# Kernel optimization log

Measured on AMD Instinct MI355X. Metric: run time of the kernel, lower is better.

The kernel has to match this reference:

```python
import jax, jax.numpy as jnp
import numpy as np

H = 16          # heads_num
D = 1024        # model_dim
HD = D // H     # per-head dim
NEG = -1e9


def setup_inputs() -> dict:
    key = jax.random.key(0)
    ks = jax.random.split(key, 12)
    B, S = 4, 1024
    inp = {
        "q": jax.random.normal(ks[0], (B, S, D), jnp.float32),
        "k": jax.random.normal(ks[1], (B, S, D), jnp.float32),
        "v": jax.random.normal(ks[2], (B, S, D), jnp.float32),
        "mask": jnp.ones((B, 1, S), jnp.int32),
    }
    s = 1.0 / np.sqrt(D)
    inp["Wq"] = jax.random.normal(ks[3], (D, D), jnp.float32) * s
    inp["bq"] = jnp.zeros((D,), jnp.float32)
    inp["Wk"] = jax.random.normal(ks[4], (D, D), jnp.float32) * s
    inp["bk"] = jnp.zeros((D,), jnp.float32)
    inp["Wv"] = jax.random.normal(ks[5], (D, D), jnp.float32) * s
    inp["bv"] = jnp.zeros((D,), jnp.float32)
    inp["Wo"] = jax.random.normal(ks[6], (D, D), jnp.float32) * s
    inp["bo"] = jnp.zeros((D,), jnp.float32)
    return inp


def _split_heads(x, B):
    # [B, S, D] -> [B, H, S, HD]
    return x.reshape(B, -1, H, HD).transpose(0, 2, 1, 3)


def reference(q, k, v, mask, Wq, bq, Wk, bk, Wv, bv, Wo, bo):
    B = q.shape[0]
    qh = _split_heads(q @ Wq.T + bq, B)  # [B,H,Sq,HD]
    kh = _split_heads(k @ Wk.T + bk, B)  # [B,H,Sk,HD]
    vh = _split_heads(v @ Wv.T + bv, B)  # [B,H,Sk,HD]
    scores = jnp.einsum("bhqd,bhkd->bhqk", qh, kh) / np.sqrt(HD)
    # mask [B,1,Sk] -> unsqueeze head dim -> [B,1,1,Sk], broadcast over q and heads
    scores = jnp.where(mask[:, None] == 0, NEG, scores)
    attn = jax.nn.softmax(scores, axis=-1)  # dropout in eval mode = identity
    ctx = jnp.einsum("bhqk,bhkd->bhqd", attn, vh)
    out = ctx.transpose(0, 2, 1, 3).reshape(B, -1, D)
    return out @ Wo.T + bo
```

## Files before the change

kernel.cpp:

```cpp
#include <hip/hip_runtime.h>
#include <hip/hip_bf16.h>
#include <math.h>

typedef __bf16 bf16;
typedef __bf16 bf16x8 __attribute__((ext_vector_type(8)));
typedef __bf16 bf16x2 __attribute__((ext_vector_type(2)));
typedef float f32x4 __attribute__((ext_vector_type(4)));
typedef float f32x16 __attribute__((ext_vector_type(16)));

#define D_MODEL 1024
#define SEQ 1024
#define BATCH 4
#define NHEAD 16
#define MTOT (BATCH*SEQ)

#define QSCALE 0.18033688011112042f
#define MASKNEG -1e9f

__global__ void cast_all(const float* __restrict__ s0, const float* __restrict__ s1,
                         const float* __restrict__ s2, const float* __restrict__ s3,
                         const float* __restrict__ s4, const float* __restrict__ s5,
                         const float* __restrict__ s6,
                         bf16* d0, bf16* d1, bf16* d2, bf16* d3, bf16* d4, bf16* d5, bf16* d6) {
    int z = blockIdx.y;
    const float* s; bf16* d; int n;
    switch (z) {
        case 0: s = s0; d = d0; n = MTOT * D_MODEL; break;
        case 1: s = s1; d = d1; n = MTOT * D_MODEL; break;
        case 2: s = s2; d = d2; n = MTOT * D_MODEL; break;
        case 3: s = s3; d = d3; n = D_MODEL * D_MODEL; break;
        case 4: s = s4; d = d4; n = D_MODEL * D_MODEL; break;
        case 5: s = s5; d = d5; n = D_MODEL * D_MODEL; break;
        default: s = s6; d = d6; n = D_MODEL * D_MODEL; break;
    }
    int idx = (blockIdx.x * blockDim.x + threadIdx.x) * 8;
    int stride = gridDim.x * blockDim.x * 8;
    for (int i = idx; i < n; i += stride) {
        const float4* p = (const float4*)(s + i);
        float4 a = p[0], b = p[1];
        bf16x8 o;
        o[0] = (bf16)a.x; o[1] = (bf16)a.y; o[2] = (bf16)a.z; o[3] = (bf16)a.w;
        o[4] = (bf16)b.x; o[5] = (bf16)b.y; o[6] = (bf16)b.z; o[7] = (bf16)b.w;
        *(bf16x8*)(d + i) = o;
    }
}

template<typename OT, int MODE>
__global__ __launch_bounds__(256, 2)
void gemm_bt(const bf16* __restrict__ A0, const bf16* __restrict__ A1, const bf16* __restrict__ A2,
             const bf16* __restrict__ W0, const bf16* __restrict__ W1, const bf16* __restrict__ W2,
             const float* __restrict__ bias0, const float* __restrict__ bias1, const float* __restrict__ bias2,
             OT* __restrict__ O0, OT* __restrict__ O1, OT* __restrict__ O2) {
    constexpr int BK = 32;
    constexpr int K = D_MODEL, N = D_MODEL;
    __shared__ alignas(16) bf16 As[128 * BK];
    __shared__ alignas(16) bf16 Bs[128 * BK];

    int z = (MODE == 0) ? blockIdx.z : 0;
    const bf16* A = (z == 0) ? A0 : (z == 1) ? A1 : A2;
    const bf16* W = (z == 0) ? W0 : (z == 1) ? W1 : W2;
    const float* bias = (z == 0) ? bias0 : (z == 1) ? bias1 : bias2;
    OT* Out = (z == 0) ? O0 : (z == 1) ? O1 : O2;

    int tid = threadIdx.x;
    int lane = tid & 63, w = tid >> 6;
    int l15 = lane & 15, l4 = lane >> 4;
    int m0 = blockIdx.x * 128;
    int n0 = blockIdx.y * 128;
    int wm = w >> 1, wn = w & 1;

    f32x4 acc[4][4] = {};

    int srow = lane >> 2;
    int scol = (lane & 3) * 8;

    for (int k0 = 0; k0 < K; k0 += BK) {
        __syncthreads();
#pragma unroll
        for (int i = 0; i < 2; ++i) {
            int seg = w * 2 + i;
            int row = seg * 16 + srow;
            const bf16* srcA = A + (size_t)(m0 + row) * K + k0 + scol;
            const bf16* srcB = W + (size_t)(n0 + row) * K + k0 + scol;
            __builtin_amdgcn_global_load_lds(
                (const __attribute__((address_space(1))) void*)srcA,
                (__attribute__((address_space(3))) void*)(As + seg * 512), 16, 0, 0);
            __builtin_amdgcn_global_load_lds(
                (const __attribute__((address_space(1))) void*)srcB,
                (__attribute__((address_space(3))) void*)(Bs + seg * 512), 16, 0, 0);
        }
        __syncthreads();

        const bf16* pa = As + (wm * 64 + l15) * BK + l4 * 8;
        const bf16* pb = Bs + (wn * 64 + l15) * BK + l4 * 8;
        bf16x8 af[4], bv[4];
#pragma unroll
        for (int m = 0; m < 4; ++m) af[m] = *(const bf16x8*)(pa + m * 16 * BK);
#pragma unroll
        for (int n = 0; n < 4; ++n) bv[n] = *(const bf16x8*)(pb + n * 16 * BK);
#pragma unroll
        for (int m = 0; m < 4; ++m)
#pragma unroll
            for (int n = 0; n < 4; ++n)
                acc[m][n] = __builtin_amdgcn_mfma_f32_16x16x32_bf16(af[m], bv[n], acc[m][n], 0, 0, 0);
    }

    float bload[4];
#pragma unroll
    for (int n = 0; n < 4; ++n) bload[n] = bias[n0 + wn * 64 + n * 16 + l15];

    if (MODE == 0 && z == 2) {
#pragma unroll
        for (int m = 0; m < 4; ++m) {
            int row = m0 + wm * 64 + m * 16 + l4 * 4;
#pragma unroll
            for (int n = 0; n < 4; ++n) {
                int col = n0 + wn * 64 + n * 16 + l15;
                float bl = bload[n];
#pragma unroll
                for (int r = 0; r < 4; ++r) {
                    float vv = acc[m][n][r] + bl;
                    int rr = row + r;
                    int bb = rr >> 10, s = rr & 1023;
                    Out[((size_t)(bb * 1024 + col)) * 1024 + s] = (OT)vv;
                }
            }
        }
    } else {
        const float sc = (MODE == 0 && z == 0) ? QSCALE : 1.0f;
#pragma unroll
        for (int m = 0; m < 4; ++m) {
            int row = m0 + wm * 64 + m * 16 + l4 * 4;
#pragma unroll
            for (int n = 0; n < 4; ++n) {
                int col = n0 + wn * 64 + n * 16 + l15;
                float bl = bload[n];
#pragma unroll
                for (int r = 0; r < 4; ++r) {
                    float vv = (acc[m][n][r] + bl) * sc;
                    Out[(size_t)(row + r) * N + col] = (OT)vv;
                }
            }
        }
    }
}

__device__ __forceinline__ unsigned pkbf(float lo, float hi2) {
    bf16x2 t; t[0] = (bf16)lo; t[1] = (bf16)hi2;
    return __builtin_bit_cast(unsigned, t);
}

__global__ __launch_bounds__(256, 2)
void attn_fwd(const bf16* __restrict__ Qp, const bf16* __restrict__ Kp,
              const bf16* __restrict__ VT, const int* __restrict__ maskp,
              bf16* __restrict__ ctx) {
    __shared__ alignas(16) bf16 Kls[2][64 * 64];
    __shared__ alignas(16) bf16 Vls[2][64 * 64];
    __shared__ alignas(16) float madd[2][64];

    int tid = threadIdx.x;
    int lane = tid & 63, w = tid >> 6;
    int l31 = lane & 31, hi = lane >> 5;

    int fid = blockIdx.x;
    int by = (fid & 7) * 8 + ((fid >> 3) >> 3);
    int bx = (fid >> 3) & 7;
    int b = by >> 4, h = by & 15;
    int q0 = bx * 128;

    bf16x8 qf[4];
    {
        const bf16* qb = Qp + ((size_t)(b * SEQ + q0 + w * 32 + l31)) * D_MODEL + h * 64 + hi * 8;
#pragma unroll
        for (int ks = 0; ks < 4; ++ks) qf[ks] = *(const bf16x8*)(qb + ks * 16);
    }

    f32x16 oacc0 = {}, oacc1 = {};
    float lsum = 0.f;

    auto stage = [&](int buf, int kt) {
        int kv0 = kt * 64;
#pragma unroll
        for (int i = 0; i < 2; ++i) {
            int seg = w * 2 + i;
            int row = seg * 8 + (lane >> 3);
            int cs = ((lane & 7) ^ (row & 7)) * 8;
            const bf16* srcK = Kp + ((size_t)(b * SEQ + kv0 + row)) * D_MODEL + h * 64 + cs;
            __builtin_amdgcn_global_load_lds(
                (const __attribute__((address_space(1))) void*)srcK,
                (__attribute__((address_space(3))) void*)(&Kls[buf][seg * 512]), 16, 0, 0);
            const bf16* srcV = VT + ((size_t)(b * 1024 + h * 64 + row)) * SEQ + kv0 + cs;
            __builtin_amdgcn_global_load_lds(
                (const __attribute__((address_space(1))) void*)srcV,
                (__attribute__((address_space(3))) void*)(&Vls[buf][seg * 512]), 16, 0, 0);
        }
        if (tid < 64) {
            madd[buf][tid] = maskp[b * SEQ + kv0 + tid] ? 0.f : MASKNEG;
        }
    };

    stage(0, 0);
    __syncthreads();

    for (int kt = 0; kt < SEQ / 64; ++kt) {
        int cur = kt & 1;
        if (kt + 1 < SEQ / 64) stage(cur ^ 1, kt + 1);

        f32x16 p0 = {}, p1 = {};
        __builtin_amdgcn_s_setprio(1);
#pragma unroll
        for (int ks = 0; ks < 4; ++ks) {
            int slot = ((2 * ks + hi) ^ (l31 & 7)) * 8;
            bf16x8 k0 = *(const bf16x8*)(&Kls[cur][l31 * 64 + slot]);
            bf16x8 k1 = *(const bf16x8*)(&Kls[cur][(32 + l31) * 64 + slot]);
            p0 = __builtin_amdgcn_mfma_f32_32x32x16_bf16(k0, qf[ks], p0, 0, 0, 0);
            p1 = __builtin_amdgcn_mfma_f32_32x32x16_bf16(k1, qf[ks], p1, 0, 0, 0);
        }
        __builtin_amdgcn_s_setprio(0);

        const float* mb = &madd[cur][0];
        float acc_s = 0.f;
#pragma unroll
        for (int g = 0; g < 4; ++g) {
            f32x4 mk0 = *(const f32x4*)(mb + g * 8 + hi * 4);
            f32x4 mk1 = *(const f32x4*)(mb + 32 + g * 8 + hi * 4);
            float s0 = 0.f, s1 = 0.f;
#pragma unroll
            for (int c = 0; c < 4; ++c) {
                int r = g * 4 + c;
                float e0 = exp2f(p0[r] + mk0[c]);
                float e1 = exp2f(p1[r] + mk1[c]);
                p0[r] = e0; p1[r] = e1;
                s0 += e0; s1 += e1;
            }
            acc_s += s0 + s1;
        }
        acc_s += __shfl_xor(acc_s, 32);
        lsum += acc_s;

        union FragU { bf16x8 v; unsigned u[4]; };
        FragU pa0, pa1, pa2, pa3;
#define PKSW(PV, RA, RB, DST)  { \
            unsigned a_ = pkbf(PV[RA], PV[(RA) + 1]); \
            unsigned b_ = pkbf(PV[RB], PV[(RB) + 1]); \
            auto rr_ = __builtin_amdgcn_permlane32_swap(a_, b_, false, false); \
            DST.u[((RA) & 3) >> 1] = rr_[0]; DST.u[(((RA) & 3) >> 1) + 2] = rr_[1]; }
        PKSW(p0, 0, 4,  pa0);
        PKSW(p0, 2, 6,  pa0);
        PKSW(p0, 8, 12, pa1);
        PKSW(p0, 10, 14, pa1);
        PKSW(p1, 0, 4,  pa2);
        PKSW(p1, 2, 6,  pa2);
        PKSW(p1, 8, 12, pa3);
        PKSW(p1, 10, 14, pa3);
#undef PKSW

        __builtin_amdgcn_s_setprio(1);
#pragma unroll
        for (int ks = 0; ks < 4; ++ks) {
            bf16x8 pav = (ks == 0) ? pa0.v : (ks == 1) ? pa1.v : (ks == 2) ? pa2.v : pa3.v;
            int slot = ((2 * ks + hi) ^ (l31 & 7)) * 8;
            bf16x8 v0 = *(const bf16x8*)(&Vls[cur][l31 * 64 + slot]);
            bf16x8 v1 = *(const bf16x8*)(&Vls[cur][(32 + l31) * 64 + slot]);
            oacc0 = __builtin_amdgcn_mfma_f32_32x32x16_bf16(pav, v0, oacc0, 0, 0, 0);
            oacc1 = __builtin_amdgcn_mfma_f32_32x32x16_bf16(pav, v1, oacc1, 0, 0, 0);
        }
        __builtin_amdgcn_s_setprio(0);

        __syncthreads();
    }

#pragma unroll
    for (int g = 0; g < 4; ++g) {
#pragma unroll
        for (int c = 0; c < 4; ++c) {
            int r = g * 4 + c;
            int qloc = c + g * 8 + hi * 4;
            float sden = __shfl(lsum, qloc);
            float inv = 1.0f / sden;
            int qg = q0 + w * 32 + qloc;
            size_t base = ((size_t)(b * SEQ + qg)) * D_MODEL + h * 64;
            ctx[base + l31]      = (bf16)(oacc0[r] * inv);
            ctx[base + 32 + l31] = (bf16)(oacc1[r] * inv);
        }
    }
}

extern "C" void kernel_launch(void* const* d_in, const int* in_sizes, int n_in,
                              void* d_out, int out_size, void* d_ws, size_t ws_size,
                              hipStream_t stream) {
    const float* q  = (const float*)d_in[0];
    const float* k  = (const float*)d_in[1];
    const float* v  = (const float*)d_in[2];
    const int* mask = (const int*)d_in[3];
    const float* Wq = (const float*)d_in[4];
    const float* bq = (const float*)d_in[5];
    const float* Wk = (const float*)d_in[6];
    const float* bk = (const float*)d_in[7];
    const float* Wv = (const float*)d_in[8];
    const float* bv = (const float*)d_in[9];
    const float* Wo = (const float*)d_in[10];
    const float* bo = (const float*)d_in[11];
    float* out = (float*)d_out;

    char* ws = (char*)d_ws;
    size_t szQKV = (size_t)MTOT * D_MODEL * sizeof(bf16);
    size_t szW = (size_t)D_MODEL * D_MODEL * sizeof(bf16);
    bf16* qb  = (bf16*)ws; ws += szQKV;
    bf16* kb  = (bf16*)ws; ws += szQKV;
    bf16* vb  = (bf16*)ws; ws += szQKV;
    bf16* Wqb = (bf16*)ws; ws += szW;
    bf16* Wkb = (bf16*)ws; ws += szW;
    bf16* Wvb = (bf16*)ws; ws += szW;
    bf16* Wob = (bf16*)ws; ws += szW;
    bf16* Qp  = (bf16*)ws; ws += szQKV;
    bf16* Kp  = (bf16*)ws; ws += szQKV;
    bf16* VT  = (bf16*)ws; ws += szQKV;
    bf16* ctx = (bf16*)ws; ws += szQKV;

    dim3 gc(512, 7, 1);
    cast_all<<<gc, 256, 0, stream>>>(q, k, v, Wq, Wk, Wv, Wo,
                                     qb, kb, vb, Wqb, Wkb, Wvb, Wob);

    dim3 g1(MTOT / 128, D_MODEL / 128, 3);
    gemm_bt<bf16, 0><<<g1, 256, 0, stream>>>(qb, kb, vb, Wqb, Wkb, Wvb,
                                             bq, bk, bv, Qp, Kp, VT);

    attn_fwd<<<dim3(512), 256, 0, stream>>>(Qp, Kp, VT, mask, ctx);

    dim3 g3(MTOT / 128, D_MODEL / 128, 1);
    gemm_bt<float, 1><<<g3, 256, 0, stream>>>(ctx, ctx, ctx, Wob, Wob, Wob,
                                              bo, bo, bo, out, out, out);
}
```

Measured before the change: 111.5 us.

## Double-buffer GEMM K-loop, widen attention blocks, skip mask add for unmasked tiles

The projection GEMM now double-buffers its LDS tiles, so the next K slice loads while MFMAs run on the current one. This drops one barrier per iteration, and the launch bounds are raised to 3 blocks per CU. The attention kernel moves to 512-thread blocks covering 256 queries, halving the grid and sharing each K/V tile across 8 waves. It also precomputes the whole mask row once per block with per-tile all-ones flags, so fully unmasked tiles skip the mask add. The trade-offs are more LDS use and register pressure, plus an added prologue pass over the mask.

```diff
diff --git a/kernel.cpp b/kernel.cpp
--- a/kernel.cpp
+++ b/kernel.cpp
@@ -46,15 +46,16 @@
 }
 
 template<typename OT, int MODE>
-__global__ __launch_bounds__(256, 2)
+__global__ __launch_bounds__(256, 3)
 void gemm_bt(const bf16* __restrict__ A0, const bf16* __restrict__ A1, const bf16* __restrict__ A2,
              const bf16* __restrict__ W0, const bf16* __restrict__ W1, const bf16* __restrict__ W2,
              const float* __restrict__ bias0, const float* __restrict__ bias1, const float* __restrict__ bias2,
              OT* __restrict__ O0, OT* __restrict__ O1, OT* __restrict__ O2) {
     constexpr int BK = 32;
-    constexpr int K = D_MODEL, N = D_MODEL;
-    __shared__ alignas(16) bf16 As[128 * BK];
-    __shared__ alignas(16) bf16 Bs[128 * BK];
+    constexpr int K = D_MODEL;
+    constexpr int NT = K / BK;
+    __shared__ alignas(16) bf16 As[2][128 * BK];
+    __shared__ alignas(16) bf16 Bs[2][128 * BK];
 
     int z = (MODE == 0) ? blockIdx.z : 0;
     const bf16* A = (z == 0) ? A0 : (z == 1) ? A1 : A2;
@@ -74,25 +75,31 @@
     int srow = lane >> 2;
     int scol = (lane & 3) * 8;
 
-    for (int k0 = 0; k0 < K; k0 += BK) {
-        __syncthreads();
+    auto stage = [&](int buf, int kt) {
 #pragma unroll
         for (int i = 0; i < 2; ++i) {
             int seg = w * 2 + i;
             int row = seg * 16 + srow;
-            const bf16* srcA = A + (size_t)(m0 + row) * K + k0 + scol;
-            const bf16* srcB = W + (size_t)(n0 + row) * K + k0 + scol;
+            const bf16* srcA = A + (size_t)(m0 + row) * K + kt * BK + scol;
+            const bf16* srcB = W + (size_t)(n0 + row) * K + kt * BK + scol;
             __builtin_amdgcn_global_load_lds(
                 (const __attribute__((address_space(1))) void*)srcA,
-                (__attribute__((address_space(3))) void*)(As + seg * 512), 16, 0, 0);
+                (__attribute__((address_space(3))) void*)(&As[buf][seg * 512]), 16, 0, 0);
             __builtin_amdgcn_global_load_lds(
                 (const __attribute__((address_space(1))) void*)srcB,
-                (__attribute__((address_space(3))) void*)(Bs + seg * 512), 16, 0, 0);
-        }
-        __syncthreads();
-
-        const bf16* pa = As + (wm * 64 + l15) * BK + l4 * 8;
-        const bf16* pb = Bs + (wn * 64 + l15) * BK + l4 * 8;
+                (__attribute__((address_space(3))) void*)(&Bs[buf][seg * 512]), 16, 0, 0);
+        }
+    };
+
+    stage(0, 0);
+    __syncthreads();
+
+    for (int kt = 0; kt < NT; ++kt) {
+        int cur = kt & 1;
+        if (kt + 1 < NT) stage(cur ^ 1, kt + 1);
+
+        const bf16* pa = &As[cur][(wm * 64 + l15) * BK + l4 * 8];
+        const bf16* pb = &Bs[cur][(wn * 64 + l15) * BK + l4 * 8];
         bf16x8 af[4], bv[4];
 #pragma unroll
         for (int m = 0; m < 4; ++m) af[m] = *(const bf16x8*)(pa + m * 16 * BK);
@@ -103,6 +110,8 @@
 #pragma unroll
             for (int n = 0; n < 4; ++n)
                 acc[m][n] = __builtin_amdgcn_mfma_f32_16x16x32_bf16(af[m], bv[n], acc[m][n], 0, 0, 0);
+
+        __syncthreads();
     }
 
     float bload[4];
@@ -138,7 +147,7 @@
 #pragma unroll
                 for (int r = 0; r < 4; ++r) {
                     float vv = (acc[m][n][r] + bl) * sc;
-                    Out[(size_t)(row + r) * N + col] = (OT)vv;
+                    Out[(size_t)(row + r) * D_MODEL + col] = (OT)vv;
                 }
             }
         }
@@ -150,23 +159,38 @@
     return __builtin_bit_cast(unsigned, t);
 }
 
-__global__ __launch_bounds__(256, 2)
+__global__ __launch_bounds__(512, 2)
 void attn_fwd(const bf16* __restrict__ Qp, const bf16* __restrict__ Kp,
               const bf16* __restrict__ VT, const int* __restrict__ maskp,
               bf16* __restrict__ ctx) {
     __shared__ alignas(16) bf16 Kls[2][64 * 64];
     __shared__ alignas(16) bf16 Vls[2][64 * 64];
-    __shared__ alignas(16) float madd[2][64];
+    __shared__ alignas(16) float madd2[SEQ];
+    __shared__ int tflag[16];
 
     int tid = threadIdx.x;
     int lane = tid & 63, w = tid >> 6;
     int l31 = lane & 31, hi = lane >> 5;
 
     int fid = blockIdx.x;
-    int by = (fid & 7) * 8 + ((fid >> 3) >> 3);
-    int bx = (fid >> 3) & 7;
+    int xcd = fid & 7, idx = fid >> 3;
+    int by = xcd * 8 + (idx >> 2);
+    int bx = idx & 3;
     int b = by >> 4, h = by & 15;
-    int q0 = bx * 128;
+    int q0 = bx * 256;
+
+    {
+        int m0v = maskp[b * SEQ + tid];
+        int m1v = maskp[b * SEQ + 512 + tid];
+        madd2[tid] = m0v ? 0.f : MASKNEG;
+        madd2[512 + tid] = m1v ? 0.f : MASKNEG;
+        unsigned long long b0 = __ballot(m0v != 0);
+        unsigned long long b1 = __ballot(m1v != 0);
+        if (lane == 0) {
+            tflag[w] = (b0 == ~0ull);
+            tflag[8 + w] = (b1 == ~0ull);
+        }
+    }
 
     bf16x8 qf[4];
     {
@@ -180,23 +204,16 @@
 
     auto stage = [&](int buf, int kt) {
         int kv0 = kt * 64;
-#pragma unroll
-        for (int i = 0; i < 2; ++i) {
-            int seg = w * 2 + i;
-            int row = seg * 8 + (lane >> 3);
-            int cs = ((lane & 7) ^ (row & 7)) * 8;
-            const bf16* srcK = Kp + ((size_t)(b * SEQ + kv0 + row)) * D_MODEL + h * 64 + cs;
-            __builtin_amdgcn_global_load_lds(
-                (const __attribute__((address_space(1))) void*)srcK,
-                (__attribute__((address_space(3))) void*)(&Kls[buf][seg * 512]), 16, 0, 0);
-            const bf16* srcV = VT + ((size_t)(b * 1024 + h * 64 + row)) * SEQ + kv0 + cs;
-            __builtin_amdgcn_global_load_lds(
-                (const __attribute__((address_space(1))) void*)srcV,
-                (__attribute__((address_space(3))) void*)(&Vls[buf][seg * 512]), 16, 0, 0);
-        }
-        if (tid < 64) {
-            madd[buf][tid] = maskp[b * SEQ + kv0 + tid] ? 0.f : MASKNEG;
-        }
+        int row = w * 8 + (lane >> 3);
+        int cs = ((lane & 7) ^ (row & 7)) * 8;
+        const bf16* srcK = Kp + ((size_t)(b * SEQ + kv0 + row)) * D_MODEL + h * 64 + cs;
+        __builtin_amdgcn_global_load_lds(
+            (const __attribute__((address_space(1))) void*)srcK,
+            (__attribute__((address_space(3))) void*)(&Kls[buf][w * 512]), 16, 0, 0);
+        const bf16* srcV = VT + ((size_t)(b * 1024 + h * 64 + row)) * SEQ + kv0 + cs;
+        __builtin_amdgcn_global_load_lds(
+            (const __attribute__((address_space(1))) void*)srcV,
+            (__attribute__((address_space(3))) void*)(&Vls[buf][w * 512]), 16, 0, 0);
     };
 
     stage(0, 0);
@@ -218,23 +235,46 @@
         }
         __builtin_amdgcn_s_setprio(0);
 
-        const float* mb = &madd[cur][0];
-        float acc_s = 0.f;
-#pragma unroll
-        for (int g = 0; g < 4; ++g) {
-            f32x4 mk0 = *(const f32x4*)(mb + g * 8 + hi * 4);
-            f32x4 mk1 = *(const f32x4*)(mb + 32 + g * 8 + hi * 4);
-            float s0 = 0.f, s1 = 0.f;
-#pragma unroll
-            for (int c = 0; c < 4; ++c) {
-                int r = g * 4 + c;
-                float e0 = exp2f(p0[r] + mk0[c]);
-                float e1 = exp2f(p1[r] + mk1[c]);
-                p0[r] = e0; p1[r] = e1;
-                s0 += e0; s1 += e1;
+        float a0 = 0.f, a1 = 0.f, a2 = 0.f, a3 = 0.f;
+        if (tflag[kt]) {
+#pragma unroll
+            for (int g = 0; g < 4; ++g) {
+                float s0 = 0.f, s1 = 0.f;
+#pragma unroll
+                for (int c = 0; c < 4; ++c) {
+                    int r = g * 4 + c;
+                    float e0 = exp2f(p0[r]);
+                    float e1 = exp2f(p1[r]);
+                    p0[r] = e0; p1[r] = e1;
+                    s0 += e0; s1 += e1;
+                }
+                if (g == 0) a0 = s0 + s1;
+                else if (g == 1) a1 = s0 + s1;
+                else if (g == 2) a2 = s0 + s1;
+                else a3 = s0 + s1;
             }
-            acc_s += s0 + s1;
-        }
+        } else {
+            const float* mb = &madd2[kt * 64];
+#pragma unroll
+            for (int g = 0; g < 4; ++g) {
+                f32x4 mk0 = *(const f32x4*)(mb + g * 8 + hi * 4);
+                f32x4 mk1 = *(const f32x4*)(mb + 32 + g * 8 + hi * 4);
+                float s0 = 0.f, s1 = 0.f;
+#pragma unroll
+                for (int c = 0; c < 4; ++c) {
+                    int r = g * 4 + c;
+                    float e0 = exp2f(p0[r] + mk0[c]);
+                    float e1 = exp2f(p1[r] + mk1[c]);
+                    p0[r] = e0; p1[r] = e1;
+                    s0 += e0; s1 += e1;
+                }
+                if (g == 0) a0 = s0 + s1;
+                else if (g == 1) a1 = s0 + s1;
+                else if (g == 2) a2 = s0 + s1;
+                else a3 = s0 + s1;
+            }
+        }
+        float acc_s = (a0 + a1) + (a2 + a3);
         acc_s += __shfl_xor(acc_s, 32);
         lsum += acc_s;
 
@@ -326,7 +366,7 @@
     gemm_bt<bf16, 0><<<g1, 256, 0, stream>>>(qb, kb, vb, Wqb, Wkb, Wvb,
                                              bq, bk, bv, Qp, Kp, VT);
 
-    attn_fwd<<<dim3(512), 256, 0, stream>>>(Qp, Kp, VT, mask, ctx);
+    attn_fwd<<<dim3(256), 512, 0, stream>>>(Qp, Kp, VT, mask, ctx);
 
     dim3 g3(MTOT / 128, D_MODEL / 128, 1);
     gemm_bt<float, 1><<<g3, 256, 0, stream>>>(ctx, ctx, ctx, Wob, Wob, Wob,
```

Result: slower. 114.2 us (+2.4%).
